# Optimization experiments

Measured on AMD Instinct MI355X. Metric: run time of the kernel, lower is better.

The kernel has to match this reference:

```python
import jax, jax.numpy as jnp
import numpy as np

E = 2  # expand_ratio


def _linear_scan(u, a):
    """h_t = a_t * h_{t-1} + u_t along axis 0, h_{-1}=0. Parallel associative scan."""
    def comb(x, y):
        a1, b1 = x
        a2, b2 = y
        return a2 * a1, a2 * b1 + b2
    _, h = jax.lax.associative_scan(comb, (a, u), axis=0)
    return h


def setup_inputs() -> dict:
    key = jax.random.key(0)
    ks = jax.random.split(key, 8)
    n, b, d = 2048, 4, 1024
    s = 1.0 / np.sqrt(d)
    return {
        "x": jax.random.normal(ks[0], (n, b, d), jnp.float32),
        "lower_bound": jax.random.uniform(ks[1], (d,), jnp.float32),
        "W_in": jax.random.normal(ks[2], (d, 3 * d), jnp.float32) * s,
        "b_in": jnp.zeros((3 * d,), jnp.float32),
        "W_out": jax.random.normal(ks[3], (d, d), jnp.float32) * s,
        "b_out": jnp.zeros((d,), jnp.float32),
        "gamma": jnp.ones((d,), jnp.float32),
        "beta": jnp.zeros((d,), jnp.float32),
    }


def reference(x, lower_bound, W_in, b_in, W_out, b_out, gamma, beta):
    n, b, d = x.shape
    h = d // E
    feat = x @ W_in + b_in                      # (n,b,3d)
    inp, og, fg = jnp.split(feat, 3, axis=-1)
    inp = jax.nn.silu(inp)
    og = jax.nn.sigmoid(og)
    fg = jax.nn.sigmoid(fg)
    # reshape (h d) -> h, d=E
    inp = inp.reshape(n, b, h, E)
    og = og.reshape(n, b, h, E)
    fg = fg.reshape(n, b, h, E)
    lb = lower_bound.reshape(h, E)
    lam = lb + (1.0 - lb) * fg                  # (n,b,h,E)
    # outer-product input: (1-lam) outer inp over the E dims -> (n,b,h,E,E)
    u = jnp.einsum('nbhd,nbhe->nbhde', 1.0 - lam, inp)
    a = jnp.broadcast_to(lam[..., None], u.shape)
    u = u.reshape(n, b, h * E * E)
    a = a.reshape(n, b, h * E * E)
    state_fwd = _linear_scan(u, a)
    state_rev = jnp.flip(_linear_scan(jnp.flip(u, 0), jnp.flip(a, 0)), 0)
    state = (state_fwd + state_rev).reshape(n, b, h, E, E)
    out = jnp.einsum('nbhde,nbhd->nbhe', state, og).reshape(n, b, d)
    # layernorm over last dim
    mu = jnp.mean(out, axis=-1, keepdims=True)
    var = jnp.var(out, axis=-1, keepdims=True)
    out = (out - mu) * jax.lax.rsqrt(var + 1e-5) * gamma + beta
    return out @ W_out + b_out
```

## Files before the change

### kernel.cpp

```cpp
#include <hip/hip_runtime.h>

typedef __bf16 bf16x8 __attribute__((ext_vector_type(8)));
typedef float floatx4 __attribute__((ext_vector_type(4)));

#define NCH 128
#define CLEN 16

__device__ __forceinline__ unsigned short f2bf(float f) {
  unsigned int u = __builtin_bit_cast(unsigned int, f);
  u += 0x7fff + ((u >> 16) & 1);
  return (unsigned short)(u >> 16);
}
__device__ __forceinline__ float bf2f(unsigned short u) {
  unsigned int v = (unsigned int)u << 16;
  return __builtin_bit_cast(float, v);
}
__device__ __forceinline__ float bf2f_lo(unsigned int u) {
  return __builtin_bit_cast(float, u << 16);
}
__device__ __forceinline__ float bf2f_hi(unsigned int u) {
  return __builtin_bit_cast(float, u & 0xffff0000u);
}

__device__ __forceinline__ void async_copy16(const void* g, void* l) {
  __builtin_amdgcn_global_load_lds(
      (const __attribute__((address_space(1))) unsigned int*)g,
      (__attribute__((address_space(3))) unsigned int*)l, 16, 0, 0);
}

__global__ void cast_x_kernel(const float* __restrict__ in, unsigned short* __restrict__ out) {
  int i = blockIdx.x * blockDim.x + threadIdx.x;
  float4 v = ((const float4*)in)[i];
  ushort4 o;
  o.x = f2bf(v.x); o.y = f2bf(v.y); o.z = f2bf(v.z); o.w = f2bf(v.w);
  ((ushort4*)out)[i] = o;
}

__global__ void tcast2_kernel(const float* __restrict__ Win, unsigned short* __restrict__ winT,
                              const float* __restrict__ Wout, unsigned short* __restrict__ woutT) {
  __shared__ float tile[32][33];
  int bx = blockIdx.x;
  const float* W;
  unsigned short* WT;
  int ncols, n0;
  if (bx < 96) { W = Win; WT = winT; ncols = 3072; n0 = bx * 32; }
  else { W = Wout; WT = woutT; ncols = 1024; n0 = (bx - 96) * 32; }
  int k0 = blockIdx.y * 32;
  int tx = threadIdx.x, ty = threadIdx.y;
  tile[ty][tx] = W[(size_t)(k0 + ty) * ncols + n0 + tx];
  __syncthreads();
  WT[(size_t)(n0 + ty) * 1024 + k0 + tx] = f2bf(tile[tx][ty]);
}

template <int EPI>
__global__ __launch_bounds__(256) void gemm_kernel(
    const unsigned short* __restrict__ A, const unsigned short* __restrict__ BT,
    const float* __restrict__ bias, const float* __restrict__ lb,
    float* __restrict__ outf,
    unsigned short* __restrict__ o_inp, unsigned short* __restrict__ o_og,
    unsigned short* __restrict__ o_om) {
  __shared__ alignas(16) char smem_raw[17408];
  unsigned short* As = (unsigned short*)smem_raw;
  unsigned short* Bs = As + 128 * 32;
  const int m0 = blockIdx.x * 128, n0 = blockIdx.y * 128;
  const int tid = threadIdx.x;
  const int lane = tid & 63, wave = tid >> 6;
  const int wm = (wave >> 1) * 64, wn = (wave & 1) * 64;
  const int mrow = lane & 15, q = lane >> 4;
  const int qsw = q ^ ((mrow >> 1) & 3);
  floatx4 acc[4][4] = {};
  const int r0 = wave * 32;
  const int srow = r0 + (lane >> 2);
  const int qs = (lane & 3) ^ ((srow >> 1) & 3);
  const unsigned short* gA0 = A + (size_t)(m0 + srow) * 1024 + qs * 8;
  const unsigned short* gA1 = gA0 + (size_t)16 * 1024;
  const unsigned short* gB0 = BT + (size_t)(n0 + srow) * 1024 + qs * 8;
  const unsigned short* gB1 = gB0 + (size_t)16 * 1024;
  unsigned short* lA0 = &As[r0 * 32];
  unsigned short* lA1 = &As[(r0 + 16) * 32];
  unsigned short* lB0 = &Bs[r0 * 32];
  unsigned short* lB1 = &Bs[(r0 + 16) * 32];
  for (int kt = 0; kt < 1024; kt += 32) {
    __syncthreads();
    async_copy16(gA0, lA0);
    async_copy16(gA1, lA1);
    async_copy16(gB0, lB0);
    async_copy16(gB1, lB1);
    gA0 += 32; gA1 += 32; gB0 += 32; gB1 += 32;
    __syncthreads();
    bf16x8 af[4], bf[4];
#pragma unroll
    for (int i = 0; i < 4; i++) af[i] = *(const bf16x8*)&As[(wm + i * 16 + mrow) * 32 + qsw * 8];
#pragma unroll
    for (int j = 0; j < 4; j++) bf[j] = *(const bf16x8*)&Bs[(wn + j * 16 + mrow) * 32 + qsw * 8];
#pragma unroll
    for (int i = 0; i < 4; i++)
#pragma unroll
      for (int j = 0; j < 4; j++)
        acc[i][j] = __builtin_amdgcn_mfma_f32_16x16x32_bf16(af[i], bf[j], acc[i][j], 0, 0, 0);
  }
  const int er = tid >> 3;
  const int ec = (tid & 7) * 16;
  const int rgbase = m0 + (er & 15) + (er >> 4) * 64;
  const int lr = (wm ? 16 : 0) + q * 4;
  float bi[4];
  int cidx[4];
#pragma unroll
  for (int j = 0; j < 4; j++) {
    cidx[j] = n0 + wn + j * 16 + mrow;
    bi[j] = bias[cidx[j]];
  }
  if (EPI == 1) {
    unsigned short* Cs = (unsigned short*)smem_raw;
    const int seg = n0 >> 10;
    unsigned short* dst = (seg == 0) ? o_inp : (seg == 1) ? o_og : o_om;
    float Lv[4];
    if (seg == 2) {
#pragma unroll
      for (int j = 0; j < 4; j++) Lv[j] = lb[cidx[j] & 1023];
    }
#pragma unroll
    for (int i = 0; i < 4; i++) {
      __syncthreads();
#pragma unroll
      for (int j = 0; j < 4; j++) {
        const int lc = wn + j * 16 + mrow;
#pragma unroll
        for (int g = 0; g < 4; g++) {
          float v = acc[i][j][g] + bi[j];
          unsigned short ob;
          if (seg == 0) { float s = 1.f / (1.f + __expf(-v)); ob = f2bf(v * s); }
          else if (seg == 1) { float s = 1.f / (1.f + __expf(-v)); ob = f2bf(s); }
          else { float sm = 1.f / (1.f + __expf(v)); ob = f2bf((1.f - Lv[j]) * sm); }
          Cs[(lr + g) * 136 + lc] = ob;
        }
      }
      __syncthreads();
      uint4 v0 = *(uint4*)&Cs[er * 136 + ec];
      uint4 v1 = *(uint4*)&Cs[er * 136 + ec + 8];
      size_t ro = (size_t)(rgbase + i * 16) * 1024 + (n0 & 1023) + ec;
      *(uint4*)&dst[ro] = v0;
      *(uint4*)&dst[ro + 8] = v1;
    }
  } else {
    float* Cf = (float*)smem_raw;
#pragma unroll
    for (int i = 0; i < 4; i++) {
      __syncthreads();
#pragma unroll
      for (int j = 0; j < 4; j++) {
        const int lc = wn + j * 16 + mrow;
#pragma unroll
        for (int g = 0; g < 4; g++) Cf[(lr + g) * 132 + lc] = acc[i][j][g] + bi[j];
      }
      __syncthreads();
      size_t ro = (size_t)(rgbase + i * 16) * 1024 + n0 + ec;
#pragma unroll
      for (int k = 0; k < 4; k++) {
        float4 v = *(float4*)&Cf[er * 132 + ec + k * 4];
        *(float4*)&outf[ro + k * 4] = v;
      }
    }
  }
}

__global__ void scan_passA(const unsigned short* __restrict__ om, const unsigned short* __restrict__ ip,
                           float* __restrict__ sumA, float* __restrict__ sumBf,
                           float* __restrict__ sumBr) {
  int idx = blockIdx.x * 256 + threadIdx.x;
  int h = idx & 511, cb = idx >> 9, b = cb & 3, c = cb >> 2;
  long base = ((long)c * CLEN * 4 + b) * 1024 + 2 * h;
  float p0 = 1.f, p1 = 1.f;
  float s00 = 0.f, s01 = 0.f, s10 = 0.f, s11 = 0.f;
  float r00 = 0.f, r01 = 0.f, r10 = 0.f, r11 = 0.f;
#pragma unroll
  for (int t = 0; t < CLEN; t++) {
    ushort2 l2 = *(const ushort2*)(om + base);
    ushort2 i2 = *(const ushort2*)(ip + base);
    base += 4096;
    float omx = bf2f(l2.x), omy = bf2f(l2.y);
    float ipx = bf2f(i2.x), ipy = bf2f(i2.y);
    float lx = 1.f - omx, ly = 1.f - omy;
    float u00 = omx * ipx, u01 = omx * ipy, u10 = omy * ipx, u11 = omy * ipy;
    r00 += p0 * u00; r01 += p0 * u01; r10 += p1 * u10; r11 += p1 * u11;
    s00 = lx * s00 + u00; s01 = lx * s01 + u01;
    s10 = ly * s10 + u10; s11 = ly * s11 + u11;
    p0 *= lx; p1 *= ly;
  }
  ((float2*)sumA)[idx] = make_float2(p0, p1);
  ((float4*)sumBf)[idx] = make_float4(s00, s01, s10, s11);
  ((float4*)sumBr)[idx] = make_float4(r00, r01, r10, r11);
}

__global__ void scan_passB(const float* __restrict__ sumA, const float* __restrict__ sumBf,
                           const float* __restrict__ sumBr, float* __restrict__ initF,
                           float* __restrict__ initR) {
  int tid = blockIdx.x * 256 + threadIdx.x;
  int dir = tid >> 13;
  int rem = tid & 8191;
  int ch = rem & 3;
  int bh = rem >> 2;
  int dd = ch >> 1;
  if (dir == 0) {
    float H = 0.f;
    for (int c = 0; c < NCH; c++) {
      int si = c * 2048 + bh;
      initF[(size_t)si * 4 + ch] = H;
      H = sumA[(size_t)si * 2 + dd] * H + sumBf[(size_t)si * 4 + ch];
    }
  } else {
    float G = 0.f;
    for (int c = NCH - 1; c >= 0; c--) {
      int si = c * 2048 + bh;
      initR[(size_t)si * 4 + ch] = G;
      G = sumA[(size_t)si * 2 + dd] * G + sumBr[(size_t)si * 4 + ch];
    }
  }
}

__global__ __launch_bounds__(512) void scanC_ln_kernel(
    const unsigned short* __restrict__ om, const unsigned short* __restrict__ ip,
    const unsigned short* __restrict__ og,
    const float* __restrict__ initF, const float* __restrict__ initR,
    const float* __restrict__ gamma, const float* __restrict__ beta,
    unsigned short* __restrict__ ybf) {
  __shared__ float tile[8][1024];
  __shared__ float ldsG[1024];
  __shared__ float ldsB[1024];
  const int h = threadIdx.x;
  const int cb = blockIdx.x;
  const int b = cb & 3, c = cb >> 2;
  const int idx = cb * 512 + h;
  *(float2*)&ldsG[2 * h] = *(const float2*)(gamma + 2 * h);
  *(float2*)&ldsB[2 * h] = *(const float2*)(beta + 2 * h);
  float4 F = ((const float4*)initF)[idx];
  float4 R = ((const float4*)initR)[idx];
  float outx[CLEN], outy[CLEN];
  unsigned int lS[CLEN], iS[CLEN], oS[CLEN];
  const long base = ((long)c * CLEN * 4 + b) * 1024 + 2 * h;
  float h00 = F.x, h01 = F.y, h10 = F.z, h11 = F.w;
  long p = base;
#pragma unroll
  for (int t = 0; t < CLEN; t++) {
    unsigned int l2 = *(const unsigned int*)(om + p);
    unsigned int i2 = *(const unsigned int*)(ip + p);
    unsigned int o2 = *(const unsigned int*)(og + p);
    p += 4096;
    lS[t] = l2; iS[t] = i2; oS[t] = o2;
    float omx = bf2f_lo(l2), omy = bf2f_hi(l2);
    float ipx = bf2f_lo(i2), ipy = bf2f_hi(i2);
    float ox = bf2f_lo(o2), oy = bf2f_hi(o2);
    float lx = 1.f - omx, ly = 1.f - omy;
    h00 = lx * h00 + omx * ipx; h01 = lx * h01 + omx * ipy;
    h10 = ly * h10 + omy * ipx; h11 = ly * h11 + omy * ipy;
    outx[t] = h00 * ox + h10 * oy;
    outy[t] = h01 * ox + h11 * oy;
  }
  float g00 = R.x, g01 = R.y, g10 = R.z, g11 = R.w;
#pragma unroll
  for (int t = CLEN - 1; t >= 0; t--) {
    unsigned int l2 = lS[t], i2 = iS[t], o2 = oS[t];
    float omx = bf2f_lo(l2), omy = bf2f_hi(l2);
    float ipx = bf2f_lo(i2), ipy = bf2f_hi(i2);
    float ox = bf2f_lo(o2), oy = bf2f_hi(o2);
    float lx = 1.f - omx, ly = 1.f - omy;
    g00 = omx * ipx + lx * g00; g01 = omx * ipy + lx * g01;
    g10 = omy * ipx + ly * g10; g11 = omy * ipy + ly * g11;
    outx[t] += g00 * ox + g10 * oy;
    outy[t] += g01 * ox + g11 * oy;
  }
  const int lane = h & 63, wv = h >> 6;
#pragma unroll
  for (int g = 0; g < CLEN / 8; g++) {
    __syncthreads();
#pragma unroll
    for (int r = 0; r < 8; r++) {
      float2 v2 = make_float2(outx[g * 8 + r], outy[g * 8 + r]);
      *(float2*)&tile[r][2 * h] = v2;
    }
    __syncthreads();
    {
      const int t = g * 8 + wv;
      float4 v[4];
#pragma unroll
      for (int k = 0; k < 4; k++) v[k] = *(const float4*)&tile[wv][lane * 16 + k * 4];
      float s = 0.f, s2 = 0.f;
#pragma unroll
      for (int k = 0; k < 4; k++) {
        s += v[k].x + v[k].y + v[k].z + v[k].w;
        s2 += v[k].x * v[k].x + v[k].y * v[k].y + v[k].z * v[k].z + v[k].w * v[k].w;
      }
#pragma unroll
      for (int off = 1; off < 64; off <<= 1) {
        s += __shfl_xor(s, off);
        s2 += __shfl_xor(s2, off);
      }
      float mean = s * (1.f / 1024.f);
      float var = s2 * (1.f / 1024.f) - mean * mean;
      float rstd = rsqrtf(var + 1e-5f);
      unsigned short o16[16];
#pragma unroll
      for (int k = 0; k < 4; k++) {
        float* vv = (float*)&v[k];
#pragma unroll
        for (int e = 0; e < 4; e++) {
          int ch = lane * 16 + k * 4 + e;
          o16[k * 4 + e] = f2bf((vv[e] - mean) * rstd * ldsG[ch] + ldsB[ch]);
        }
      }
      size_t rowo = ((size_t)(c * CLEN + t) * 4 + b) * 1024 + lane * 16;
      *(uint4*)(ybf + rowo) = *(uint4*)&o16[0];
      *(uint4*)(ybf + rowo + 8) = *(uint4*)&o16[8];
    }
  }
}

extern "C" void kernel_launch(void* const* d_in, const int* in_sizes, int n_in,
                              void* d_out, int out_size, void* d_ws, size_t ws_size,
                              hipStream_t stream) {
  const float* x = (const float*)d_in[0];
  const float* lb = (const float*)d_in[1];
  const float* Win = (const float*)d_in[2];
  const float* bin = (const float*)d_in[3];
  const float* Wout = (const float*)d_in[4];
  const float* bout = (const float*)d_in[5];
  const float* gamma = (const float*)d_in[6];
  const float* beta = (const float*)d_in[7];
  float* out = (float*)d_out;

  char* ws = (char*)d_ws;
  size_t off = 0;
  auto alloc = [&](size_t bytes) {
    void* p = ws + off;
    off += (bytes + 255) & ~(size_t)255;
    return p;
  };
  unsigned short* x_bf = (unsigned short*)alloc(8192ull * 1024 * 2);
  unsigned short* winT = (unsigned short*)alloc(3072ull * 1024 * 2);
  unsigned short* woutT = (unsigned short*)alloc(1024ull * 1024 * 2);
  unsigned short* inp_b = (unsigned short*)alloc(8192ull * 1024 * 2);
  unsigned short* og_b = (unsigned short*)alloc(8192ull * 1024 * 2);
  unsigned short* om_b = (unsigned short*)alloc(8192ull * 1024 * 2);
  unsigned short* y_bf = (unsigned short*)alloc(8192ull * 1024 * 2);
  float* sumA = (float*)alloc((size_t)NCH * 4 * 512 * 2 * 4);
  float* sumBf = (float*)alloc((size_t)NCH * 4 * 512 * 4 * 4);
  float* sumBr = (float*)alloc((size_t)NCH * 4 * 512 * 4 * 4);
  float* initF = (float*)alloc((size_t)NCH * 4 * 512 * 4 * 4);
  float* initR = (float*)alloc((size_t)NCH * 4 * 512 * 4 * 4);

  cast_x_kernel<<<8192, 256, 0, stream>>>(x, x_bf);
  tcast2_kernel<<<dim3(128, 32), dim3(32, 32), 0, stream>>>(Win, winT, Wout, woutT);
  gemm_kernel<1><<<dim3(64, 24), 256, 0, stream>>>(x_bf, winT, bin, lb, nullptr, inp_b, og_b, om_b);
  scan_passA<<<(NCH * 4 * 512) / 256, 256, 0, stream>>>(om_b, inp_b, sumA, sumBf, sumBr);
  scan_passB<<<64, 256, 0, stream>>>(sumA, sumBf, sumBr, initF, initR);
  scanC_ln_kernel<<<NCH * 4, 512, 0, stream>>>(om_b, inp_b, og_b, initF, initR, gamma, beta, y_bf);
  gemm_kernel<0><<<dim3(64, 8), 256, 0, stream>>>(y_bf, woutT, bout, nullptr, out, nullptr, nullptr, nullptr);
}
```

Baseline: 243.1 us.

## Fuse chunked scan passes into one cooperative kernel and merge prep casts

Merges the x cast and the weight transpose-casts into a single prep kernel, and fuses the three scan passes (chunk summaries, cross-chunk carry propagation, final scan plus layernorm) into one cooperative kernel with two grid-wide syncs. The aim is to remove kernel launch overhead and inter-kernel gaps. In exchange, the carry pass runs on only 64 threads per block, the final pass is serialised over two chunk-batches per block, and correctness depends on all 256 blocks being co-resident.

New measurement: 404.4 us. 1.66x slower.

```diff
diff --git a/kernel.cpp b/kernel.cpp
--- a/kernel.cpp
+++ b/kernel.cpp
@@ -1,4 +1,5 @@
 #include <hip/hip_runtime.h>
+#include <hip/hip_cooperative_groups.h>
 
 typedef __bf16 bf16x8 __attribute__((ext_vector_type(8)));
 typedef float floatx4 __attribute__((ext_vector_type(4)));
@@ -28,28 +29,41 @@
       (__attribute__((address_space(3))) unsigned int*)l, 16, 0, 0);
 }
 
-__global__ void cast_x_kernel(const float* __restrict__ in, unsigned short* __restrict__ out) {
-  int i = blockIdx.x * blockDim.x + threadIdx.x;
-  float4 v = ((const float4*)in)[i];
-  ushort4 o;
-  o.x = f2bf(v.x); o.y = f2bf(v.y); o.z = f2bf(v.z); o.w = f2bf(v.w);
-  ((ushort4*)out)[i] = o;
-}
-
-__global__ void tcast2_kernel(const float* __restrict__ Win, unsigned short* __restrict__ winT,
-                              const float* __restrict__ Wout, unsigned short* __restrict__ woutT) {
+__global__ __launch_bounds__(256) void prep_kernel(
+    const float* __restrict__ x, unsigned short* __restrict__ x_bf,
+    const float* __restrict__ Win, unsigned short* __restrict__ winT,
+    const float* __restrict__ Wout, unsigned short* __restrict__ woutT) {
   __shared__ float tile[32][33];
   int bx = blockIdx.x;
-  const float* W;
-  unsigned short* WT;
-  int ncols, n0;
-  if (bx < 96) { W = Win; WT = winT; ncols = 3072; n0 = bx * 32; }
-  else { W = Wout; WT = woutT; ncols = 1024; n0 = (bx - 96) * 32; }
-  int k0 = blockIdx.y * 32;
-  int tx = threadIdx.x, ty = threadIdx.y;
-  tile[ty][tx] = W[(size_t)(k0 + ty) * ncols + n0 + tx];
-  __syncthreads();
-  WT[(size_t)(n0 + ty) * 1024 + k0 + tx] = f2bf(tile[tx][ty]);
+  int tid = threadIdx.x;
+  if (bx < 8192) {
+    int i = bx * 256 + tid;
+    float4 v = ((const float4*)x)[i];
+    ushort4 o;
+    o.x = f2bf(v.x); o.y = f2bf(v.y); o.z = f2bf(v.z); o.w = f2bf(v.w);
+    ((ushort4*)x_bf)[i] = o;
+  } else {
+    int tb = bx - 8192;
+    int nt = tb & 127, kt = tb >> 7;
+    const float* W;
+    unsigned short* WT;
+    int ncols, n0;
+    if (nt < 96) { W = Win; WT = winT; ncols = 3072; n0 = nt * 32; }
+    else { W = Wout; WT = woutT; ncols = 1024; n0 = (nt - 96) * 32; }
+    int k0 = kt * 32;
+    int tx = tid & 31, ty8 = tid >> 5;
+#pragma unroll
+    for (int r = 0; r < 4; r++) {
+      int ty = ty8 + r * 8;
+      tile[ty][tx] = W[(size_t)(k0 + ty) * ncols + n0 + tx];
+    }
+    __syncthreads();
+#pragma unroll
+    for (int r = 0; r < 4; r++) {
+      int ty = ty8 + r * 8;
+      WT[(size_t)(n0 + ty) * 1024 + k0 + tx] = f2bf(tile[tx][ty]);
+    }
+  }
 }
 
 template <int EPI>
@@ -164,122 +178,129 @@
   }
 }
 
-__global__ void scan_passA(const unsigned short* __restrict__ om, const unsigned short* __restrict__ ip,
-                           float* __restrict__ sumA, float* __restrict__ sumBf,
-                           float* __restrict__ sumBr) {
-  int idx = blockIdx.x * 256 + threadIdx.x;
-  int h = idx & 511, cb = idx >> 9, b = cb & 3, c = cb >> 2;
-  long base = ((long)c * CLEN * 4 + b) * 1024 + 2 * h;
-  float p0 = 1.f, p1 = 1.f;
-  float s00 = 0.f, s01 = 0.f, s10 = 0.f, s11 = 0.f;
-  float r00 = 0.f, r01 = 0.f, r10 = 0.f, r11 = 0.f;
-#pragma unroll
-  for (int t = 0; t < CLEN; t++) {
-    ushort2 l2 = *(const ushort2*)(om + base);
-    ushort2 i2 = *(const ushort2*)(ip + base);
-    base += 4096;
-    float omx = bf2f(l2.x), omy = bf2f(l2.y);
-    float ipx = bf2f(i2.x), ipy = bf2f(i2.y);
-    float lx = 1.f - omx, ly = 1.f - omy;
-    float u00 = omx * ipx, u01 = omx * ipy, u10 = omy * ipx, u11 = omy * ipy;
-    r00 += p0 * u00; r01 += p0 * u01; r10 += p1 * u10; r11 += p1 * u11;
-    s00 = lx * s00 + u00; s01 = lx * s01 + u01;
-    s10 = ly * s10 + u10; s11 = ly * s11 + u11;
-    p0 *= lx; p1 *= ly;
-  }
-  ((float2*)sumA)[idx] = make_float2(p0, p1);
-  ((float4*)sumBf)[idx] = make_float4(s00, s01, s10, s11);
-  ((float4*)sumBr)[idx] = make_float4(r00, r01, r10, r11);
-}
-
-__global__ void scan_passB(const float* __restrict__ sumA, const float* __restrict__ sumBf,
-                           const float* __restrict__ sumBr, float* __restrict__ initF,
-                           float* __restrict__ initR) {
-  int tid = blockIdx.x * 256 + threadIdx.x;
-  int dir = tid >> 13;
-  int rem = tid & 8191;
-  int ch = rem & 3;
-  int bh = rem >> 2;
-  int dd = ch >> 1;
-  if (dir == 0) {
-    float H = 0.f;
-    for (int c = 0; c < NCH; c++) {
-      int si = c * 2048 + bh;
-      initF[(size_t)si * 4 + ch] = H;
-      H = sumA[(size_t)si * 2 + dd] * H + sumBf[(size_t)si * 4 + ch];
-    }
-  } else {
-    float G = 0.f;
-    for (int c = NCH - 1; c >= 0; c--) {
-      int si = c * 2048 + bh;
-      initR[(size_t)si * 4 + ch] = G;
-      G = sumA[(size_t)si * 2 + dd] * G + sumBr[(size_t)si * 4 + ch];
-    }
-  }
-}
-
-__global__ __launch_bounds__(512) void scanC_ln_kernel(
+__global__ __launch_bounds__(512, 2) void scan_mid_kernel(
     const unsigned short* __restrict__ om, const unsigned short* __restrict__ ip,
     const unsigned short* __restrict__ og,
-    const float* __restrict__ initF, const float* __restrict__ initR,
+    float* __restrict__ sumA, float* __restrict__ sumBf, float* __restrict__ sumBr,
+    float* __restrict__ initF, float* __restrict__ initR,
     const float* __restrict__ gamma, const float* __restrict__ beta,
     unsigned short* __restrict__ ybf) {
   __shared__ float tile[8][1024];
   __shared__ float ldsG[1024];
   __shared__ float ldsB[1024];
   const int h = threadIdx.x;
-  const int cb = blockIdx.x;
-  const int b = cb & 3, c = cb >> 2;
-  const int idx = cb * 512 + h;
   *(float2*)&ldsG[2 * h] = *(const float2*)(gamma + 2 * h);
   *(float2*)&ldsB[2 * h] = *(const float2*)(beta + 2 * h);
-  float4 F = ((const float4*)initF)[idx];
-  float4 R = ((const float4*)initR)[idx];
-  float outx[CLEN], outy[CLEN];
-  unsigned int lS[CLEN], iS[CLEN], oS[CLEN];
-  const long base = ((long)c * CLEN * 4 + b) * 1024 + 2 * h;
-  float h00 = F.x, h01 = F.y, h10 = F.z, h11 = F.w;
-  long p = base;
-#pragma unroll
-  for (int t = 0; t < CLEN; t++) {
-    unsigned int l2 = *(const unsigned int*)(om + p);
-    unsigned int i2 = *(const unsigned int*)(ip + p);
-    unsigned int o2 = *(const unsigned int*)(og + p);
-    p += 4096;
-    lS[t] = l2; iS[t] = i2; oS[t] = o2;
-    float omx = bf2f_lo(l2), omy = bf2f_hi(l2);
-    float ipx = bf2f_lo(i2), ipy = bf2f_hi(i2);
-    float ox = bf2f_lo(o2), oy = bf2f_hi(o2);
-    float lx = 1.f - omx, ly = 1.f - omy;
-    h00 = lx * h00 + omx * ipx; h01 = lx * h01 + omx * ipy;
-    h10 = ly * h10 + omy * ipx; h11 = ly * h11 + omy * ipy;
-    outx[t] = h00 * ox + h10 * oy;
-    outy[t] = h01 * ox + h11 * oy;
-  }
-  float g00 = R.x, g01 = R.y, g10 = R.z, g11 = R.w;
-#pragma unroll
-  for (int t = CLEN - 1; t >= 0; t--) {
-    unsigned int l2 = lS[t], i2 = iS[t], o2 = oS[t];
-    float omx = bf2f_lo(l2), omy = bf2f_hi(l2);
-    float ipx = bf2f_lo(i2), ipy = bf2f_hi(i2);
-    float ox = bf2f_lo(o2), oy = bf2f_hi(o2);
-    float lx = 1.f - omx, ly = 1.f - omy;
-    g00 = omx * ipx + lx * g00; g01 = omx * ipy + lx * g01;
-    g10 = omy * ipx + ly * g10; g11 = omy * ipy + ly * g11;
-    outx[t] += g00 * ox + g10 * oy;
-    outy[t] += g01 * ox + g11 * oy;
-  }
+
+#pragma unroll
+  for (int rep = 0; rep < 2; rep++) {
+    const int cb = blockIdx.x + rep * 256;
+    const int b = cb & 3, c = cb >> 2;
+    const int idx = cb * 512 + h;
+    long base = ((long)c * CLEN * 4 + b) * 1024 + 2 * h;
+    float p0 = 1.f, p1 = 1.f;
+    float s00 = 0.f, s01 = 0.f, s10 = 0.f, s11 = 0.f;
+    float r00 = 0.f, r01 = 0.f, r10 = 0.f, r11 = 0.f;
+#pragma unroll
+    for (int t = 0; t < CLEN; t++) {
+      unsigned int l2 = *(const unsigned int*)(om + base);
+      unsigned int i2 = *(const unsigned int*)(ip + base);
+      base += 4096;
+      float omx = bf2f_lo(l2), omy = bf2f_hi(l2);
+      float ipx = bf2f_lo(i2), ipy = bf2f_hi(i2);
+      float lx = 1.f - omx, ly = 1.f - omy;
+      float u00 = omx * ipx, u01 = omx * ipy, u10 = omy * ipx, u11 = omy * ipy;
+      r00 += p0 * u00; r01 += p0 * u01; r10 += p1 * u10; r11 += p1 * u11;
+      s00 = lx * s00 + u00; s01 = lx * s01 + u01;
+      s10 = ly * s10 + u10; s11 = ly * s11 + u11;
+      p0 *= lx; p1 *= ly;
+    }
+    ((float2*)sumA)[idx] = make_float2(p0, p1);
+    ((float4*)sumBf)[idx] = make_float4(s00, s01, s10, s11);
+    ((float4*)sumBr)[idx] = make_float4(r00, r01, r10, r11);
+  }
+  __threadfence();
+  cooperative_groups::this_grid().sync();
+
+  if (h < 64) {
+    int tid = blockIdx.x * 64 + h;
+    int dir = tid >> 13;
+    int rem = tid & 8191;
+    int ch = rem & 3;
+    int bh = rem >> 2;
+    int dd = ch >> 1;
+    if (dir == 0) {
+      float H = 0.f;
+#pragma unroll 4
+      for (int c = 0; c < NCH; c++) {
+        int si = c * 2048 + bh;
+        initF[(size_t)si * 4 + ch] = H;
+        H = sumA[(size_t)si * 2 + dd] * H + sumBf[(size_t)si * 4 + ch];
+      }
+    } else {
+      float G = 0.f;
+#pragma unroll 4
+      for (int c = NCH - 1; c >= 0; c--) {
+        int si = c * 2048 + bh;
+        initR[(size_t)si * 4 + ch] = G;
+        G = sumA[(size_t)si * 2 + dd] * G + sumBr[(size_t)si * 4 + ch];
+      }
+    }
+  }
+  __threadfence();
+  cooperative_groups::this_grid().sync();
+
   const int lane = h & 63, wv = h >> 6;
-#pragma unroll
-  for (int g = 0; g < CLEN / 8; g++) {
-    __syncthreads();
-#pragma unroll
-    for (int r = 0; r < 8; r++) {
-      float2 v2 = make_float2(outx[g * 8 + r], outy[g * 8 + r]);
-      *(float2*)&tile[r][2 * h] = v2;
-    }
-    __syncthreads();
-    {
+#pragma unroll 1
+  for (int rep = 0; rep < 2; rep++) {
+    const int cb = blockIdx.x + rep * 256;
+    const int b = cb & 3, c = cb >> 2;
+    const int idx = cb * 512 + h;
+    float4 F = ((const float4*)initF)[idx];
+    float4 R = ((const float4*)initR)[idx];
+    float outx[CLEN], outy[CLEN];
+    unsigned int lS[CLEN], iS[CLEN], oS[CLEN];
+    const long base = ((long)c * CLEN * 4 + b) * 1024 + 2 * h;
+    float h00 = F.x, h01 = F.y, h10 = F.z, h11 = F.w;
+    long p = base;
+#pragma unroll
+    for (int t = 0; t < CLEN; t++) {
+      unsigned int l2 = *(const unsigned int*)(om + p);
+      unsigned int i2 = *(const unsigned int*)(ip + p);
+      unsigned int o2 = *(const unsigned int*)(og + p);
+      p += 4096;
+      lS[t] = l2; iS[t] = i2; oS[t] = o2;
+      float omx = bf2f_lo(l2), omy = bf2f_hi(l2);
+      float ipx = bf2f_lo(i2), ipy = bf2f_hi(i2);
+      float ox = bf2f_lo(o2), oy = bf2f_hi(o2);
+      float lx = 1.f - omx, ly = 1.f - omy;
+      h00 = lx * h00 + omx * ipx; h01 = lx * h01 + omx * ipy;
+      h10 = ly * h10 + omy * ipx; h11 = ly * h11 + omy * ipy;
+      outx[t] = h00 * ox + h10 * oy;
+      outy[t] = h01 * ox + h11 * oy;
+    }
+    float g00 = R.x, g01 = R.y, g10 = R.z, g11 = R.w;
+#pragma unroll
+    for (int t = CLEN - 1; t >= 0; t--) {
+      unsigned int l2 = lS[t], i2 = iS[t], o2 = oS[t];
+      float omx = bf2f_lo(l2), omy = bf2f_hi(l2);
+      float ipx = bf2f_lo(i2), ipy = bf2f_hi(i2);
+      float ox = bf2f_lo(o2), oy = bf2f_hi(o2);
+      float lx = 1.f - omx, ly = 1.f - omy;
+      g00 = omx * ipx + lx * g00; g01 = omx * ipy + lx * g01;
+      g10 = omy * ipx + ly * g10; g11 = omy * ipy + ly * g11;
+      outx[t] += g00 * ox + g10 * oy;
+      outy[t] += g01 * ox + g11 * oy;
+    }
+#pragma unroll
+    for (int g = 0; g < CLEN / 8; g++) {
+      __syncthreads();
+#pragma unroll
+      for (int r = 0; r < 8; r++) {
+        float2 v2 = make_float2(outx[g * 8 + r], outy[g * 8 + r]);
+        *(float2*)&tile[r][2 * h] = v2;
+      }
+      __syncthreads();
       const int t = g * 8 + wv;
       float4 v[4];
 #pragma unroll
@@ -312,6 +333,7 @@
       *(uint4*)(ybf + rowo) = *(uint4*)&o16[0];
       *(uint4*)(ybf + rowo + 8) = *(uint4*)&o16[8];
     }
+    __syncthreads();
   }
 }
 
@@ -348,11 +370,22 @@
   float* initF = (float*)alloc((size_t)NCH * 4 * 512 * 4 * 4);
   float* initR = (float*)alloc((size_t)NCH * 4 * 512 * 4 * 4);
 
-  cast_x_kernel<<<8192, 256, 0, stream>>>(x, x_bf);
-  tcast2_kernel<<<dim3(128, 32), dim3(32, 32), 0, stream>>>(Win, winT, Wout, woutT);
+  prep_kernel<<<12288, 256, 0, stream>>>(x, x_bf, Win, winT, Wout, woutT);
   gemm_kernel<1><<<dim3(64, 24), 256, 0, stream>>>(x_bf, winT, bin, lb, nullptr, inp_b, og_b, om_b);
-  scan_passA<<<(NCH * 4 * 512) / 256, 256, 0, stream>>>(om_b, inp_b, sumA, sumBf, sumBr);
-  scan_passB<<<64, 256, 0, stream>>>(sumA, sumBf, sumBr, initF, initR);
-  scanC_ln_kernel<<<NCH * 4, 512, 0, stream>>>(om_b, inp_b, og_b, initF, initR, gamma, beta, y_bf);
+  {
+    const unsigned short* a_om = om_b;
+    const unsigned short* a_ip = inp_b;
+    const unsigned short* a_og = og_b;
+    float* a_sumA = sumA; float* a_sumBf = sumBf; float* a_sumBr = sumBr;
+    float* a_initF = initF; float* a_initR = initR;
+    const float* a_gamma = gamma; const float* a_beta = beta;
+    unsigned short* a_y = y_bf;
+    void* args[] = {(void*)&a_om, (void*)&a_ip, (void*)&a_og,
+                    (void*)&a_sumA, (void*)&a_sumBf, (void*)&a_sumBr,
+                    (void*)&a_initF, (void*)&a_initR,
+                    (void*)&a_gamma, (void*)&a_beta, (void*)&a_y};
+    hipLaunchCooperativeKernel((const void*)scan_mid_kernel, dim3(256), dim3(512),
+                               args, 0, stream);
+  }
   gemm_kernel<0><<<dim3(64, 8), 256, 0, stream>>>(y_bf, woutT, bout, nullptr, out, nullptr, nullptr, nullptr);
 }
```
